# Kernel tuning notes

Measured on AMD Instinct MI355X. Metric: run time of the kernel, lower is better.

## Reference

```python
import jax, jax.numpy as jnp
import numpy as np

D_MODEL = 2048
NUM_HEADS = 16
HEAD_DIM = D_MODEL // NUM_HEADS
D_FF = 4 * D_MODEL
B, L = 2, 2048
LN_EPS = 1e-6


def layer_norm(x, scale, bias):
    x32 = x.astype(jnp.float32)
    mu = jnp.mean(x32, axis=-1, keepdims=True)
    var = jnp.mean(jnp.square(x32 - mu), axis=-1, keepdims=True)
    return (x32 - mu) * jax.lax.rsqrt(var + LN_EPS) * scale + bias


def setup_inputs() -> dict:
    key = jax.random.key(0)
    ks = jax.random.split(key, 10)
    s = 1.0 / np.sqrt(D_MODEL)
    x = jax.random.normal(ks[0], (B, L, D_MODEL), dtype=jnp.float32)
    mask = jnp.tril(jnp.ones((L, L), dtype=bool))[None, None, :, :]  # causal [1,1,L,L]
    wq = jax.random.normal(ks[1], (D_MODEL, D_MODEL), jnp.float32) * s
    wk = jax.random.normal(ks[2], (D_MODEL, D_MODEL), jnp.float32) * s
    wv = jax.random.normal(ks[3], (D_MODEL, D_MODEL), jnp.float32) * s
    wo = jax.random.normal(ks[4], (D_MODEL, D_MODEL), jnp.float32) * s
    w1 = jax.random.normal(ks[5], (D_MODEL, D_FF), jnp.float32) * s
    b1 = jnp.zeros((D_FF,), jnp.float32)
    w2 = jax.random.normal(ks[6], (D_FF, D_MODEL), jnp.float32) * (1.0 / np.sqrt(D_FF))
    b2 = jnp.zeros((D_MODEL,), jnp.float32)
    ln1_scale = jnp.ones((D_MODEL,), jnp.float32)
    ln1_bias = jnp.zeros((D_MODEL,), jnp.float32)
    ln2_scale = jnp.ones((D_MODEL,), jnp.float32)
    ln2_bias = jnp.zeros((D_MODEL,), jnp.float32)
    return {"x": x, "mask": mask, "ln1_scale": ln1_scale, "ln1_bias": ln1_bias,
            "wq": wq, "wk": wk, "wv": wv, "wo": wo,
            "ln2_scale": ln2_scale, "ln2_bias": ln2_bias,
            "w1": w1, "b1": b1, "w2": w2, "b2": b2}


def reference(x, mask, ln1_scale, ln1_bias, wq, wk, wv, wo,
              ln2_scale, ln2_bias, w1, b1, w2, b2):
    residual = x
    h = layer_norm(x, ln1_scale, ln1_bias)
    b, l, _ = h.shape
    q = (h @ wq).reshape(b, l, NUM_HEADS, HEAD_DIM)
    k = (h @ wk).reshape(b, l, NUM_HEADS, HEAD_DIM)
    v = (h @ wv).reshape(b, l, NUM_HEADS, HEAD_DIM)
    scores = jnp.einsum('bqhd,bkhd->bhqk', q, k) / jnp.sqrt(jnp.float32(HEAD_DIM))
    scores = jnp.where(mask, scores, -100000.0)
    attn = jax.nn.softmax(scores, axis=-1)
    attn_out = jnp.einsum('bhqk,bkhd->bqhd', attn, v).reshape(b, l, D_MODEL)
    x = residual + attn_out @ wo
    mlp = jax.nn.gelu(layer_norm(x, ln2_scale, ln2_bias) @ w1 + b1)
    return x + mlp @ w2 + b2
```

## Files before the change

kernel.cpp:

```cpp
#include <hip/hip_runtime.h>
#include <hip/hip_bf16.h>

typedef unsigned short u16;
typedef __bf16 bf16x8 __attribute__((ext_vector_type(8)));
typedef float f32x4 __attribute__((ext_vector_type(4)));

#define D_MODEL 2048
#define D_FF    8192
#define NH      16
#define HD      128
#define BATCH   2
#define SEQ     2048
#define ROWS    (BATCH*SEQ)

__device__ __forceinline__ u16 f2bf(float f) {
  union { __hip_bfloat16 h; u16 u; } cv;
  cv.h = __float2bfloat16(f);
  return cv.u;
}

__device__ __forceinline__ void gload16(const u16* g, u16* l) {
  __builtin_amdgcn_global_load_lds((const __attribute__((address_space(1))) void*)g,
                                   (__attribute__((address_space(3))) void*)l,
                                   16, 0, 0);
}

__device__ __forceinline__ float gelu_f(float x) {
  const float k0 = 0.7978845608028654f, k1 = 0.044715f;
  return 0.5f * x * (1.0f + tanhf(k0 * (x + k1 * x * x * x)));
}

__global__ __launch_bounds__(256) void ln_bf16_kernel(
    const float* __restrict__ x, const float* __restrict__ sc,
    const float* __restrict__ bs, u16* __restrict__ out)
{
  __shared__ float red[8];
  const int row = blockIdx.x, t = threadIdx.x;
  const int w = t >> 6, l = t & 63;
  const float* xr = x + (size_t)row * D_MODEL;
  float4 a = ((const float4*)xr)[t*2];
  float4 b = ((const float4*)xr)[t*2+1];
  float s  = a.x+a.y+a.z+a.w + b.x+b.y+b.z+b.w;
  float s2 = a.x*a.x+a.y*a.y+a.z*a.z+a.w*a.w + b.x*b.x+b.y*b.y+b.z*b.z+b.w*b.w;
  for (int off = 32; off; off >>= 1) { s += __shfl_down(s, off); s2 += __shfl_down(s2, off); }
  if (l == 0) { red[w] = s; red[4+w] = s2; }
  __syncthreads();
  s  = red[0]+red[1]+red[2]+red[3];
  s2 = red[4]+red[5]+red[6]+red[7];
  const float mu  = s * (1.0f / D_MODEL);
  const float var = s2 * (1.0f / D_MODEL) - mu * mu;
  const float inv = rsqrtf(var + 1e-6f);
  float4 g0 = ((const float4*)sc)[t*2], g1 = ((const float4*)sc)[t*2+1];
  float4 q0 = ((const float4*)bs)[t*2], q1 = ((const float4*)bs)[t*2+1];
  union { u16 u[8]; uint4 v; } o;
  o.u[0] = f2bf((a.x-mu)*inv*g0.x + q0.x);
  o.u[1] = f2bf((a.y-mu)*inv*g0.y + q0.y);
  o.u[2] = f2bf((a.z-mu)*inv*g0.z + q0.z);
  o.u[3] = f2bf((a.w-mu)*inv*g0.w + q0.w);
  o.u[4] = f2bf((b.x-mu)*inv*g1.x + q1.x);
  o.u[5] = f2bf((b.y-mu)*inv*g1.y + q1.y);
  o.u[6] = f2bf((b.z-mu)*inv*g1.z + q1.z);
  o.u[7] = f2bf((b.w-mu)*inv*g1.w + q1.w);
  *(uint4*)(&out[(size_t)row * D_MODEL + t*8]) = o.v;
}

__global__ __launch_bounds__(256) void transpose_w(
    const float* __restrict__ in, u16* __restrict__ out, int R, int C)
{
  __shared__ float tile[32][33];
  const int t = threadIdx.x;
  const int c0 = blockIdx.x*32, r0 = blockIdx.y*32;
  const int col = t & 31, rb = t >> 5;
#pragma unroll
  for (int i = 0; i < 4; ++i)
    tile[rb + i*8][col] = in[(size_t)(r0 + rb + i*8)*C + c0 + col];
  __syncthreads();
#pragma unroll
  for (int i = 0; i < 4; ++i)
    out[(size_t)(c0 + rb + i*8)*R + r0 + col] = f2bf(tile[col][rb + i*8]);
}

__global__ __launch_bounds__(256) void transpose_v(
    const u16* __restrict__ qkv, u16* __restrict__ vt)
{
  __shared__ u16 tile[32][34];
  const int t = threadIdx.x;
  const int b = blockIdx.z;
  const int c0 = blockIdx.x*32, r0 = blockIdx.y*32;
  const int col = t & 31, rb = t >> 5;
  const u16* inb = qkv + (size_t)b*SEQ*3*D_MODEL + 2*D_MODEL;
#pragma unroll
  for (int i = 0; i < 4; ++i)
    tile[rb+i*8][col] = inb[(size_t)(r0+rb+i*8)*(3*D_MODEL) + c0+col];
  __syncthreads();
  u16* ob = vt + (size_t)b*SEQ*D_MODEL;
#pragma unroll
  for (int i = 0; i < 4; ++i)
    ob[(size_t)(c0+rb+i*8)*SEQ + r0+col] = tile[col][rb+i*8];
}

template<int EPI>
__global__ __launch_bounds__(256) void gemm_bt(
    const u16* __restrict__ A, const u16* __restrict__ BT,
    void* __restrict__ Cout, const float* __restrict__ bias,
    const float* __restrict__ res, int N, int K)
{
  __shared__ u16 As[128*64];
  __shared__ u16 Bs[128*64];
  const int t = threadIdx.x;
  const int m0 = blockIdx.y*128, n0 = blockIdx.x*128;
  const int l = t & 63, w = t >> 6;
  const int wr = w >> 1, wc = w & 1;
  const int l15 = l & 15, lq = l >> 4;
  f32x4 acc[4][4] = {};

  for (int kt = 0; kt < K; kt += 64) {
    __syncthreads();
#pragma unroll
    for (int i = 0; i < 4; ++i) {
      const int o16 = i*256 + t;
      const int row = o16 >> 3, cs = o16 & 7;
      const int srcc = cs ^ (row & 7);
      gload16(A  + (size_t)(m0+row)*K + kt + srcc*8, &As[o16*8]);
      gload16(BT + (size_t)(n0+row)*K + kt + srcc*8, &Bs[o16*8]);
    }
    __syncthreads();
#pragma unroll
    for (int kk = 0; kk < 2; ++kk) {
      bf16x8 af[4], bfr[4];
#pragma unroll
      for (int mi = 0; mi < 4; ++mi) {
        const int r = wr*64 + mi*16 + l15;
        af[mi] = *(const bf16x8*)&As[r*64 + ((kk*4+lq) ^ (r&7))*8];
      }
#pragma unroll
      for (int ni = 0; ni < 4; ++ni) {
        const int r = wc*64 + ni*16 + l15;
        bfr[ni] = *(const bf16x8*)&Bs[r*64 + ((kk*4+lq) ^ (r&7))*8];
      }
#pragma unroll
      for (int mi = 0; mi < 4; ++mi)
#pragma unroll
        for (int ni = 0; ni < 4; ++ni)
          acc[mi][ni] = __builtin_amdgcn_mfma_f32_16x16x32_bf16(af[mi], bfr[ni], acc[mi][ni], 0, 0, 0);
    }
  }

  const int colb = n0 + wc*64;
  const int rowb = m0 + wr*64;
#pragma unroll
  for (int mi = 0; mi < 4; ++mi) {
#pragma unroll
    for (int ni = 0; ni < 4; ++ni) {
      const int col = colb + ni*16 + l15;
      const int row0 = rowb + mi*16 + lq*4;
      float bv = 0.f;
      if (EPI == 2 || EPI == 3) bv = bias[col];
#pragma unroll
      for (int r = 0; r < 4; ++r) {
        float v = acc[mi][ni][r];
        const size_t idx = (size_t)(row0 + r) * N + col;
        if (EPI == 0)      ((u16*)Cout)[idx] = f2bf(v);
        else if (EPI == 1) ((float*)Cout)[idx] = v + res[idx];
        else if (EPI == 2) ((u16*)Cout)[idx] = f2bf(gelu_f(v + bv));
        else               ((float*)Cout)[idx] = v + bv + res[idx];
      }
    }
  }
}

__global__ __launch_bounds__(256) void attn_kernel(
    const u16* __restrict__ qkv, const u16* __restrict__ vt,
    u16* __restrict__ out)
{
  __shared__ u16 Ks[64*128];
  __shared__ u16 Vs[128*64];
  __shared__ u16 Ps[4*16*64];
  const int t = threadIdx.x;
  const int qt = blockIdx.x & 31, bh = blockIdx.x >> 5;
  const int b = bh >> 4, h = bh & 15;
  const int w = t >> 6, l = t & 63;
  const int l15 = l & 15, lq = l >> 4;

  bf16x8 qf[4];
  {
    const u16* qb = qkv + (size_t)(b*SEQ + qt*64 + w*16 + l15)*(3*D_MODEL) + h*HD;
#pragma unroll
    for (int kk = 0; kk < 4; ++kk)
      qf[kk] = *(const bf16x8*)(qb + kk*32 + lq*8);
  }
  float m[4]    = {-INFINITY, -INFINITY, -INFINITY, -INFINITY};
  float lsum[4] = {0.f, 0.f, 0.f, 0.f};
  f32x4 acc_o[8] = {};
  const size_t kbase = (size_t)b*SEQ*(3*D_MODEL) + D_MODEL + h*HD;
  const size_t vbase = (size_t)(b*SEQ + h*HD) * SEQ;
  u16* pw = &Ps[w*1024];

  for (int j = 0; j <= qt; ++j) {
    __syncthreads();
#pragma unroll
    for (int i = 0; i < 4; ++i) {
      const int o16 = i*256 + t;
      {
        const int row = o16 >> 4, cs = o16 & 15;
        const int srcc = cs ^ (row & 7);
        gload16(qkv + kbase + (size_t)(j*64+row)*(3*D_MODEL) + srcc*8, &Ks[o16*8]);
      }
      {
        const int row = o16 >> 3, cs = o16 & 7;
        const int srcc = cs ^ (row & 7);
        gload16(vt + vbase + (size_t)row*SEQ + j*64 + srcc*8, &Vs[o16*8]);
      }
    }
    __syncthreads();

    f32x4 sacc[4] = {};
#pragma unroll
    for (int nf = 0; nf < 4; ++nf) {
      const int kr = nf*16 + l15;
      const int sw = kr & 7;
#pragma unroll
      for (int kk = 0; kk < 4; ++kk) {
        bf16x8 kf = *(const bf16x8*)&Ks[kr*128 + ((kk*4+lq) ^ sw)*8];
        sacc[nf] = __builtin_amdgcn_mfma_f32_16x16x32_bf16(qf[kk], kf, sacc[nf], 0, 0, 0);
      }
    }

    const float scale = 0.08838834764831845f;
    if (j == qt) {
#pragma unroll
      for (int nf = 0; nf < 4; ++nf)
#pragma unroll
        for (int r = 0; r < 4; ++r) {
          float s = sacc[nf][r] * scale;
          const int ki = nf*16 + l15;
          const int qi = w*16 + lq*4 + r;
          if (ki > qi) s = -100000.0f;
          sacc[nf][r] = s;
        }
    } else {
#pragma unroll
      for (int nf = 0; nf < 4; ++nf)
#pragma unroll
        for (int r = 0; r < 4; ++r) sacc[nf][r] *= scale;
    }

    float scal[4];
#pragma unroll
    for (int r = 0; r < 4; ++r) {
      float mx = fmaxf(fmaxf(sacc[0][r], sacc[1][r]), fmaxf(sacc[2][r], sacc[3][r]));
#pragma unroll
      for (int off = 1; off < 16; off <<= 1)
        mx = fmaxf(mx, __shfl_xor(mx, off));
      const float mn = fmaxf(m[r], mx);
      scal[r] = __expf(m[r] - mn);
      m[r] = mn;
      float rs = 0.f;
#pragma unroll
      for (int nf = 0; nf < 4; ++nf) {
        const float p = __expf(sacc[nf][r] - mn);
        sacc[nf][r] = p;
        rs += p;
      }
#pragma unroll
      for (int off = 1; off < 16; off <<= 1)
        rs += __shfl_xor(rs, off);
      lsum[r] = lsum[r]*scal[r] + rs;
    }
#pragma unroll
    for (int nf2 = 0; nf2 < 8; ++nf2)
#pragma unroll
      for (int r = 0; r < 4; ++r) acc_o[nf2][r] *= scal[r];

#pragma unroll
    for (int nf = 0; nf < 4; ++nf)
#pragma unroll
      for (int r = 0; r < 4; ++r) {
        const int qr = lq*4 + r, kc = nf*16 + l15;
        pw[qr*64 + (((kc>>3) ^ (qr&7))*8 + (kc&7))] = f2bf(sacc[nf][r]);
      }

#pragma unroll
    for (int kk2 = 0; kk2 < 2; ++kk2) {
      bf16x8 pf = *(const bf16x8*)&pw[l15*64 + (((kk2*4+lq) ^ (l15&7))*8)];
#pragma unroll
      for (int nf2 = 0; nf2 < 8; ++nf2) {
        const int vr = nf2*16 + l15;
        bf16x8 vf = *(const bf16x8*)&Vs[vr*64 + ((kk2*4+lq) ^ (vr&7))*8];
        acc_o[nf2] = __builtin_amdgcn_mfma_f32_16x16x32_bf16(pf, vf, acc_o[nf2], 0, 0, 0);
      }
    }
  }

  const size_t ro = (size_t)(b*SEQ + qt*64 + w*16 + lq*4);
#pragma unroll
  for (int r = 0; r < 4; ++r) {
    const float inv = 1.0f / lsum[r];
#pragma unroll
    for (int nf2 = 0; nf2 < 8; ++nf2)
      out[(ro + r)*D_MODEL + h*HD + nf2*16 + l15] = f2bf(acc_o[nf2][r] * inv);
  }
}

extern "C" void kernel_launch(void* const* d_in, const int* in_sizes, int n_in,
                              void* d_out, int out_size, void* d_ws, size_t ws_size,
                              hipStream_t stream)
{
  (void)in_sizes; (void)n_in; (void)out_size; (void)ws_size;
  const float* x    = (const float*)d_in[0];
  const float* ln1s = (const float*)d_in[2];
  const float* ln1b = (const float*)d_in[3];
  const float* wq   = (const float*)d_in[4];
  const float* wk   = (const float*)d_in[5];
  const float* wv   = (const float*)d_in[6];
  const float* wo   = (const float*)d_in[7];
  const float* ln2s = (const float*)d_in[8];
  const float* ln2b = (const float*)d_in[9];
  const float* w1   = (const float*)d_in[10];
  const float* b1   = (const float*)d_in[11];
  const float* w2   = (const float*)d_in[12];
  const float* b2   = (const float*)d_in[13];
  float* out = (float*)d_out;

  char* ws = (char*)d_ws;
  constexpr size_t OFF_WQKV = 0;
  constexpr size_t OFF_WO   = OFF_WQKV + (size_t)3*D_MODEL*D_MODEL*2;
  constexpr size_t OFF_W1   = OFF_WO   + (size_t)D_MODEL*D_MODEL*2;
  constexpr size_t OFF_W2   = OFF_W1   + (size_t)D_FF*D_MODEL*2;
  constexpr size_t OFF_H    = OFF_W2   + (size_t)D_MODEL*D_FF*2;
  constexpr size_t OFF_QKV  = OFF_H    + (size_t)ROWS*D_MODEL*2;
  constexpr size_t OFF_VT   = OFF_QKV  + (size_t)ROWS*3*D_MODEL*2;
  constexpr size_t OFF_ATTN = OFF_VT   + (size_t)ROWS*D_MODEL*2;
  constexpr size_t OFF_X2   = OFF_ATTN + (size_t)ROWS*D_MODEL*2;

  u16*   wqkv_bt = (u16*)(ws + OFF_WQKV);
  u16*   wo_bt   = (u16*)(ws + OFF_WO);
  u16*   w1_bt   = (u16*)(ws + OFF_W1);
  u16*   w2_bt   = (u16*)(ws + OFF_W2);
  u16*   h_bf    = (u16*)(ws + OFF_H);
  u16*   qkv     = (u16*)(ws + OFF_QKV);
  u16*   vt      = (u16*)(ws + OFF_VT);
  u16*   act     = qkv;
  u16*   attn    = (u16*)(ws + OFF_ATTN);
  float* x2      = (float*)(ws + OFF_X2);

  const dim3 B256(256);

  transpose_w<<<dim3(64,64),  B256, 0, stream>>>(wq, wqkv_bt,                 D_MODEL, D_MODEL);
  transpose_w<<<dim3(64,64),  B256, 0, stream>>>(wk, wqkv_bt + (size_t)D_MODEL*D_MODEL,   D_MODEL, D_MODEL);
  transpose_w<<<dim3(64,64),  B256, 0, stream>>>(wv, wqkv_bt + (size_t)2*D_MODEL*D_MODEL, D_MODEL, D_MODEL);
  transpose_w<<<dim3(64,64),  B256, 0, stream>>>(wo, wo_bt, D_MODEL, D_MODEL);
  transpose_w<<<dim3(256,64), B256, 0, stream>>>(w1, w1_bt, D_MODEL, D_FF);
  transpose_w<<<dim3(64,256), B256, 0, stream>>>(w2, w2_bt, D_FF, D_MODEL);

  ln_bf16_kernel<<<ROWS, B256, 0, stream>>>(x, ln1s, ln1b, h_bf);
  gemm_bt<0><<<dim3(48,32), B256, 0, stream>>>(h_bf, wqkv_bt, qkv, nullptr, nullptr, 3*D_MODEL, D_MODEL);
  transpose_v<<<dim3(64,64,2), B256, 0, stream>>>(qkv, vt);
  attn_kernel<<<dim3(BATCH*NH*32), B256, 0, stream>>>(qkv, vt, attn);
  gemm_bt<1><<<dim3(16,32), B256, 0, stream>>>(attn, wo_bt, x2, nullptr, x, D_MODEL, D_MODEL);
  ln_bf16_kernel<<<ROWS, B256, 0, stream>>>(x2, ln2s, ln2b, h_bf);
  gemm_bt<2><<<dim3(64,32), B256, 0, stream>>>(h_bf, w1_bt, act, b1, nullptr, D_FF, D_MODEL);
  gemm_bt<3><<<dim3(16,32), B256, 0, stream>>>(act, w2_bt, out, b2, x2, D_MODEL, D_FF);
}
```

Baseline: 769.7 us.

## Replace GEMM with 256-tile multi-stage pipelined kernels and XCD-aware block remap

Replaces the single 128x128 GEMM with two variants: a 256x256 tile kernel for the QKV and W1 GEMMs and a 256x128 kernel for the Wo and W2 GEMMs. Both use 512 threads and a 4-buffer LDS ring with 3 tiles of global->LDS prefetch in flight. They split the MFMA work into halves interleaved with the loads, use explicit waitcnt/barriers and setprio around MFMA bursts, and remap block IDs across the 8 XCDs for L2 locality. The aim is to hide global-memory latency and raise arithmetic intensity per block. In exchange it uses more LDS and registers, and relies on hand-placed waitcnt counts being correct.

New measurement: 719.4 us. -6.5%, faster.

```diff
diff --git a/kernel.cpp b/kernel.cpp
--- a/kernel.cpp
+++ b/kernel.cpp
@@ -100,70 +100,200 @@
 }
 
 template<int EPI>
-__global__ __launch_bounds__(256) void gemm_bt(
+__global__ __launch_bounds__(512, 2) void gemm256(
     const u16* __restrict__ A, const u16* __restrict__ BT,
     void* __restrict__ Cout, const float* __restrict__ bias,
-    const float* __restrict__ res, int N, int K)
-{
-  __shared__ u16 As[128*64];
-  __shared__ u16 Bs[128*64];
+    int N, int K, int gridN)
+{
+  __shared__ __align__(16) u16 lds[65536];
   const int t = threadIdx.x;
-  const int m0 = blockIdx.y*128, n0 = blockIdx.x*128;
-  const int l = t & 63, w = t >> 6;
-  const int wr = w >> 1, wc = w & 1;
+  const int nwg = gridDim.x;
+  const int wg = (int)blockIdx.x;
+  const int wgid = (wg & 7) * (nwg >> 3) + (wg >> 3);
+  const int bx = wgid % gridN, by = wgid / gridN;
+  const int m0 = by * 256, n0 = bx * 256;
+  const int w = t >> 6, l = t & 63;
+  const int wm = w >> 2, wn = w & 3;
   const int l15 = l & 15, lq = l >> 4;
+
+  const int o0 = t, o1 = 512 + t;
+  const int r0 = o0 >> 2, c0s = (o0 & 3) ^ ((r0 >> 1) & 3);
+  const int r1 = o1 >> 2, c1s = (o1 & 3) ^ ((r1 >> 1) & 3);
+  const u16* a0 = A  + (size_t)(m0 + r0) * K + c0s * 8;
+  const u16* a1 = A  + (size_t)(m0 + r1) * K + c1s * 8;
+  const u16* b0 = BT + (size_t)(n0 + r0) * K + c0s * 8;
+  const u16* b1 = BT + (size_t)(n0 + r1) * K + c1s * 8;
+
+  int offA[4], offA2[4], offB[4];
+#pragma unroll
+  for (int i = 0; i < 4; ++i) {
+    const int ra  = wm * 128 + i * 16 + l15;
+    offA[i]  = ra * 32 + ((lq ^ ((ra >> 1) & 3)) * 8);
+    const int ra2 = ra + 64;
+    offA2[i] = ra2 * 32 + ((lq ^ ((ra2 >> 1) & 3)) * 8);
+    const int rb  = wn * 64 + i * 16 + l15;
+    offB[i]  = 8192 + rb * 32 + ((lq ^ ((rb >> 1) & 3)) * 8);
+  }
+
+  f32x4 acc[8][4] = {};
+  const int nt = K >> 5;
+
+#define STAGE_A(tile) { u16* d = &lds[((tile) & 3) * 16384]; \
+    gload16(a0 + (size_t)(tile) * 32, d + o0 * 8); \
+    gload16(a1 + (size_t)(tile) * 32, d + o1 * 8); }
+#define STAGE_B(tile) { u16* d = &lds[((tile) & 3) * 16384 + 8192]; \
+    gload16(b0 + (size_t)(tile) * 32, d + o0 * 8); \
+    gload16(b1 + (size_t)(tile) * 32, d + o1 * 8); }
+
+  STAGE_A(0); STAGE_B(0); STAGE_A(1); STAGE_B(1); STAGE_A(2); STAGE_B(2);
+  asm volatile("s_waitcnt vmcnt(8)" ::: "memory");
+  __builtin_amdgcn_sched_barrier(0);
+  __builtin_amdgcn_s_barrier();
+
+  for (int tt = 0; tt < nt; ++tt) {
+    u16* buf = &lds[(tt & 3) * 16384];
+    bf16x8 af[4], bfr[4];
+#pragma unroll
+    for (int i = 0; i < 4; ++i) af[i]  = *(const bf16x8*)&buf[offA[i]];
+#pragma unroll
+    for (int i = 0; i < 4; ++i) bfr[i] = *(const bf16x8*)&buf[offB[i]];
+    if (tt + 3 < nt) STAGE_A(tt + 3);
+    __builtin_amdgcn_s_barrier();
+    asm volatile("s_waitcnt lgkmcnt(0)" ::: "memory");
+    __builtin_amdgcn_sched_barrier(0);
+    __builtin_amdgcn_s_setprio(1);
+#pragma unroll
+    for (int mi = 0; mi < 4; ++mi)
+#pragma unroll
+      for (int ni = 0; ni < 4; ++ni)
+        acc[mi][ni] = __builtin_amdgcn_mfma_f32_16x16x32_bf16(af[mi], bfr[ni], acc[mi][ni], 0, 0, 0);
+    __builtin_amdgcn_s_setprio(0);
+    __builtin_amdgcn_s_barrier();
+    bf16x8 af2[4];
+#pragma unroll
+    for (int i = 0; i < 4; ++i) af2[i] = *(const bf16x8*)&buf[offA2[i]];
+    if (tt + 3 < nt) STAGE_B(tt + 3);
+    __builtin_amdgcn_s_barrier();
+    asm volatile("s_waitcnt lgkmcnt(0)" ::: "memory");
+    __builtin_amdgcn_sched_barrier(0);
+    __builtin_amdgcn_s_setprio(1);
+#pragma unroll
+    for (int mi = 0; mi < 4; ++mi)
+#pragma unroll
+      for (int ni = 0; ni < 4; ++ni)
+        acc[4 + mi][ni] = __builtin_amdgcn_mfma_f32_16x16x32_bf16(af2[mi], bfr[ni], acc[4 + mi][ni], 0, 0, 0);
+    __builtin_amdgcn_s_setprio(0);
+    asm volatile("s_waitcnt vmcnt(8)" ::: "memory");
+    __builtin_amdgcn_sched_barrier(0);
+    __builtin_amdgcn_s_barrier();
+  }
+#undef STAGE_A
+#undef STAGE_B
+
+  const int rowb = m0 + wm * 128;
+  const int colb = n0 + wn * 64;
+#pragma unroll
+  for (int mi = 0; mi < 8; ++mi) {
+#pragma unroll
+    for (int ni = 0; ni < 4; ++ni) {
+      const int col = colb + ni * 16 + l15;
+      const int row0 = rowb + mi * 16 + lq * 4;
+      float bv = (EPI == 2) ? bias[col] : 0.f;
+#pragma unroll
+      for (int r = 0; r < 4; ++r) {
+        const float v = acc[mi][ni][r];
+        const size_t idx = (size_t)(row0 + r) * N + col;
+        if (EPI == 0) ((u16*)Cout)[idx] = f2bf(v);
+        else          ((u16*)Cout)[idx] = f2bf(gelu_f(v + bv));
+      }
+    }
+  }
+}
+
+template<int EPI>
+__global__ __launch_bounds__(512, 2) void gemm128(
+    const u16* __restrict__ A, const u16* __restrict__ BT,
+    float* __restrict__ Cout, const float* __restrict__ bias,
+    const float* __restrict__ res, int N, int K, int gridN)
+{
+  __shared__ __align__(16) u16 lds[49152];
+  const int t = threadIdx.x;
+  const int nwg = gridDim.x;
+  const int wg = (int)blockIdx.x;
+  const int wgid = (wg & 7) * (nwg >> 3) + (wg >> 3);
+  const int bx = wgid % gridN, by = wgid / gridN;
+  const int m0 = by * 256, n0 = bx * 128;
+  const int w = t >> 6, l = t & 63;
+  const int wm = w >> 1, wn = w & 1;
+  const int l15 = l & 15, lq = l >> 4;
+
+  const int o0 = t, o1 = 512 + t;
+  const int r0 = o0 >> 2, c0s = (o0 & 3) ^ ((r0 >> 1) & 3);
+  const int r1 = o1 >> 2, c1s = (o1 & 3) ^ ((r1 >> 1) & 3);
+  const u16* a0 = A  + (size_t)(m0 + r0) * K + c0s * 8;
+  const u16* a1 = A  + (size_t)(m0 + r1) * K + c1s * 8;
+  const u16* bsrc = BT + (size_t)(n0 + r0) * K + c0s * 8;
+
+  int offA[4], offB[4];
+#pragma unroll
+  for (int i = 0; i < 4; ++i) {
+    const int ra = wm * 64 + i * 16 + l15;
+    offA[i] = ra * 32 + ((lq ^ ((ra >> 1) & 3)) * 8);
+    const int rb = wn * 64 + i * 16 + l15;
+    offB[i] = 8192 + rb * 32 + ((lq ^ ((rb >> 1) & 3)) * 8);
+  }
+
   f32x4 acc[4][4] = {};
-
-  for (int kt = 0; kt < K; kt += 64) {
-    __syncthreads();
-#pragma unroll
-    for (int i = 0; i < 4; ++i) {
-      const int o16 = i*256 + t;
-      const int row = o16 >> 3, cs = o16 & 7;
-      const int srcc = cs ^ (row & 7);
-      gload16(A  + (size_t)(m0+row)*K + kt + srcc*8, &As[o16*8]);
-      gload16(BT + (size_t)(n0+row)*K + kt + srcc*8, &Bs[o16*8]);
-    }
-    __syncthreads();
-#pragma unroll
-    for (int kk = 0; kk < 2; ++kk) {
-      bf16x8 af[4], bfr[4];
-#pragma unroll
-      for (int mi = 0; mi < 4; ++mi) {
-        const int r = wr*64 + mi*16 + l15;
-        af[mi] = *(const bf16x8*)&As[r*64 + ((kk*4+lq) ^ (r&7))*8];
-      }
-#pragma unroll
-      for (int ni = 0; ni < 4; ++ni) {
-        const int r = wc*64 + ni*16 + l15;
-        bfr[ni] = *(const bf16x8*)&Bs[r*64 + ((kk*4+lq) ^ (r&7))*8];
-      }
-#pragma unroll
-      for (int mi = 0; mi < 4; ++mi)
-#pragma unroll
-        for (int ni = 0; ni < 4; ++ni)
-          acc[mi][ni] = __builtin_amdgcn_mfma_f32_16x16x32_bf16(af[mi], bfr[ni], acc[mi][ni], 0, 0, 0);
-    }
-  }
-
-  const int colb = n0 + wc*64;
-  const int rowb = m0 + wr*64;
+  const int nt = K >> 5;
+
+#define STAGE(tile) { u16* d = &lds[((tile) & 3) * 12288]; \
+    gload16(a0 + (size_t)(tile) * 32, d + o0 * 8); \
+    gload16(a1 + (size_t)(tile) * 32, d + o1 * 8); \
+    gload16(bsrc + (size_t)(tile) * 32, d + 8192 + o0 * 8); }
+
+  STAGE(0); STAGE(1); STAGE(2);
+  asm volatile("s_waitcnt vmcnt(6)" ::: "memory");
+  __builtin_amdgcn_sched_barrier(0);
+  __builtin_amdgcn_s_barrier();
+
+  for (int tt = 0; tt < nt; ++tt) {
+    u16* buf = &lds[(tt & 3) * 12288];
+    bf16x8 af[4], bfr[4];
+#pragma unroll
+    for (int i = 0; i < 4; ++i) af[i]  = *(const bf16x8*)&buf[offA[i]];
+#pragma unroll
+    for (int i = 0; i < 4; ++i) bfr[i] = *(const bf16x8*)&buf[offB[i]];
+    if (tt + 3 < nt) STAGE(tt + 3);
+    __builtin_amdgcn_s_barrier();
+    asm volatile("s_waitcnt lgkmcnt(0)" ::: "memory");
+    __builtin_amdgcn_sched_barrier(0);
+    __builtin_amdgcn_s_setprio(1);
+#pragma unroll
+    for (int mi = 0; mi < 4; ++mi)
+#pragma unroll
+      for (int ni = 0; ni < 4; ++ni)
+        acc[mi][ni] = __builtin_amdgcn_mfma_f32_16x16x32_bf16(af[mi], bfr[ni], acc[mi][ni], 0, 0, 0);
+    __builtin_amdgcn_s_setprio(0);
+    asm volatile("s_waitcnt vmcnt(6)" ::: "memory");
+    __builtin_amdgcn_sched_barrier(0);
+    __builtin_amdgcn_s_barrier();
+  }
+#undef STAGE
+
+  const int rowb = m0 + wm * 64;
+  const int colb = n0 + wn * 64;
 #pragma unroll
   for (int mi = 0; mi < 4; ++mi) {
 #pragma unroll
     for (int ni = 0; ni < 4; ++ni) {
-      const int col = colb + ni*16 + l15;
-      const int row0 = rowb + mi*16 + lq*4;
-      float bv = 0.f;
-      if (EPI == 2 || EPI == 3) bv = bias[col];
+      const int col = colb + ni * 16 + l15;
+      const int row0 = rowb + mi * 16 + lq * 4;
+      float bv = (EPI == 3) ? bias[col] : 0.f;
 #pragma unroll
       for (int r = 0; r < 4; ++r) {
-        float v = acc[mi][ni][r];
+        const float v = acc[mi][ni][r];
         const size_t idx = (size_t)(row0 + r) * N + col;
-        if (EPI == 0)      ((u16*)Cout)[idx] = f2bf(v);
-        else if (EPI == 1) ((float*)Cout)[idx] = v + res[idx];
-        else if (EPI == 2) ((u16*)Cout)[idx] = f2bf(gelu_f(v + bv));
-        else               ((float*)Cout)[idx] = v + bv + res[idx];
+        Cout[idx] = v + bv + res[idx];
       }
     }
   }
@@ -344,7 +474,7 @@
   u16*   attn    = (u16*)(ws + OFF_ATTN);
   float* x2      = (float*)(ws + OFF_X2);
 
-  const dim3 B256(256);
+  const dim3 B256(256), B512(512);
 
   transpose_w<<<dim3(64,64),  B256, 0, stream>>>(wq, wqkv_bt,                 D_MODEL, D_MODEL);
   transpose_w<<<dim3(64,64),  B256, 0, stream>>>(wk, wqkv_bt + (size_t)D_MODEL*D_MODEL,   D_MODEL, D_MODEL);
@@ -354,11 +484,11 @@
   transpose_w<<<dim3(64,256), B256, 0, stream>>>(w2, w2_bt, D_FF, D_MODEL);
 
   ln_bf16_kernel<<<ROWS, B256, 0, stream>>>(x, ln1s, ln1b, h_bf);
-  gemm_bt<0><<<dim3(48,32), B256, 0, stream>>>(h_bf, wqkv_bt, qkv, nullptr, nullptr, 3*D_MODEL, D_MODEL);
+  gemm256<0><<<dim3(384), B512, 0, stream>>>(h_bf, wqkv_bt, qkv, nullptr, 3*D_MODEL, D_MODEL, 24);
   transpose_v<<<dim3(64,64,2), B256, 0, stream>>>(qkv, vt);
   attn_kernel<<<dim3(BATCH*NH*32), B256, 0, stream>>>(qkv, vt, attn);
-  gemm_bt<1><<<dim3(16,32), B256, 0, stream>>>(attn, wo_bt, x2, nullptr, x, D_MODEL, D_MODEL);
+  gemm128<1><<<dim3(256), B512, 0, stream>>>(attn, wo_bt, x2, nullptr, x, D_MODEL, D_MODEL, 16);
   ln_bf16_kernel<<<ROWS, B256, 0, stream>>>(x2, ln2s, ln2b, h_bf);
-  gemm_bt<2><<<dim3(64,32), B256, 0, stream>>>(h_bf, w1_bt, act, b1, nullptr, D_FF, D_MODEL);
-  gemm_bt<3><<<dim3(16,32), B256, 0, stream>>>(act, w2_bt, out, b2, x2, D_MODEL, D_FF);
-}
+  gemm256<2><<<dim3(512), B512, 0, stream>>>(h_bf, w1_bt, act, b1, D_FF, D_MODEL, 32);
+  gemm128<3><<<dim3(256), B512, 0, stream>>>(act, w2_bt, out, b2, x2, D_MODEL, D_FF, 16);
+}
```

## Pipeline GEMM with four-stage LDS ring buffer and XCD-aware block remapping

Applied to the files above, without the earlier changes.

Replaces the single-buffered 128x128x64 GEMM with a 4-deep LDS ring of 32-wide K tiles. Loads are issued three tiles ahead and gated by vmcnt waits, so global loads overlap the MFMA work. It also adds a 1D grid with block-id remapping across the 8 XCDs for L2 locality, setprio around the MFMAs, and 2 blocks per CU via launch bounds. The cost is more LDS per block (64KB), which may limit occupancy, and delicate barrier and waitcnt ordering.

New measurement: 772.7 us. Within noise of the previous version (+0.4%).

```diff
diff --git a/kernel.cpp b/kernel.cpp
--- a/kernel.cpp
+++ b/kernel.cpp
@@ -100,65 +100,95 @@
 }
 
 template<int EPI>
-__global__ __launch_bounds__(256) void gemm_bt(
+__global__ __launch_bounds__(256, 2) void gemm_p4(
     const u16* __restrict__ A, const u16* __restrict__ BT,
     void* __restrict__ Cout, const float* __restrict__ bias,
-    const float* __restrict__ res, int N, int K)
-{
-  __shared__ u16 As[128*64];
-  __shared__ u16 Bs[128*64];
+    const float* __restrict__ res, int N, int K, int gridN)
+{
+  __shared__ __align__(16) u16 lds[32768];
   const int t = threadIdx.x;
-  const int m0 = blockIdx.y*128, n0 = blockIdx.x*128;
-  const int l = t & 63, w = t >> 6;
-  const int wr = w >> 1, wc = w & 1;
+  const int nwg = gridDim.x;
+  const int wg = (int)blockIdx.x;
+  const int wgid = (wg & 7) * (nwg >> 3) + (wg >> 3);
+  const int bx = wgid % gridN, by = wgid / gridN;
+  const int m0 = by * 128, n0 = bx * 128;
+  const int w = t >> 6, l = t & 63;
+  const int wm = w >> 1, wn = w & 1;
   const int l15 = l & 15, lq = l >> 4;
+
+  const int o0 = t, o1 = 256 + t;
+  const int r0 = o0 >> 2, c0s = (o0 & 3) ^ ((r0 >> 1) & 3);
+  const int r1 = o1 >> 2, c1s = (o1 & 3) ^ ((r1 >> 1) & 3);
+  const u16* a0 = A  + (size_t)(m0 + r0) * K + c0s * 8;
+  const u16* a1 = A  + (size_t)(m0 + r1) * K + c1s * 8;
+  const u16* b0 = BT + (size_t)(n0 + r0) * K + c0s * 8;
+  const u16* b1 = BT + (size_t)(n0 + r1) * K + c1s * 8;
+
+  int offA[4], offB[4];
+#pragma unroll
+  for (int i = 0; i < 4; ++i) {
+    const int ra = wm * 64 + i * 16 + l15;
+    offA[i] = ra * 32 + ((lq ^ ((ra >> 1) & 3)) * 8);
+    const int rb = wn * 64 + i * 16 + l15;
+    offB[i] = 4096 + rb * 32 + ((lq ^ ((rb >> 1) & 3)) * 8);
+  }
+
   f32x4 acc[4][4] = {};
-
-  for (int kt = 0; kt < K; kt += 64) {
-    __syncthreads();
-#pragma unroll
-    for (int i = 0; i < 4; ++i) {
-      const int o16 = i*256 + t;
-      const int row = o16 >> 3, cs = o16 & 7;
-      const int srcc = cs ^ (row & 7);
-      gload16(A  + (size_t)(m0+row)*K + kt + srcc*8, &As[o16*8]);
-      gload16(BT + (size_t)(n0+row)*K + kt + srcc*8, &Bs[o16*8]);
-    }
-    __syncthreads();
-#pragma unroll
-    for (int kk = 0; kk < 2; ++kk) {
-      bf16x8 af[4], bfr[4];
-#pragma unroll
-      for (int mi = 0; mi < 4; ++mi) {
-        const int r = wr*64 + mi*16 + l15;
-        af[mi] = *(const bf16x8*)&As[r*64 + ((kk*4+lq) ^ (r&7))*8];
-      }
-#pragma unroll
-      for (int ni = 0; ni < 4; ++ni) {
-        const int r = wc*64 + ni*16 + l15;
-        bfr[ni] = *(const bf16x8*)&Bs[r*64 + ((kk*4+lq) ^ (r&7))*8];
-      }
-#pragma unroll
-      for (int mi = 0; mi < 4; ++mi)
-#pragma unroll
-        for (int ni = 0; ni < 4; ++ni)
-          acc[mi][ni] = __builtin_amdgcn_mfma_f32_16x16x32_bf16(af[mi], bfr[ni], acc[mi][ni], 0, 0, 0);
-    }
-  }
-
-  const int colb = n0 + wc*64;
-  const int rowb = m0 + wr*64;
+  const int nt = K >> 5;
+
+#define STAGE(tile) { u16* d = &lds[((tile) & 3) * 8192]; \
+    gload16(a0 + (size_t)(tile) * 32, d + o0 * 8); \
+    gload16(a1 + (size_t)(tile) * 32, d + o1 * 8); \
+    gload16(b0 + (size_t)(tile) * 32, d + 4096 + o0 * 8); \
+    gload16(b1 + (size_t)(tile) * 32, d + 4096 + o1 * 8); }
+
+#define KSTEP(TT, DOSTAGE, VMSTR) { \
+    u16* buf = &lds[((TT) & 3) * 8192]; \
+    if (DOSTAGE) STAGE((TT) + 3); \
+    bf16x8 af[4], bfr[4]; \
+    _Pragma("unroll") \
+    for (int i = 0; i < 4; ++i) af[i]  = *(const bf16x8*)&buf[offA[i]]; \
+    _Pragma("unroll") \
+    for (int i = 0; i < 4; ++i) bfr[i] = *(const bf16x8*)&buf[offB[i]]; \
+    __builtin_amdgcn_s_barrier(); \
+    asm volatile("s_waitcnt lgkmcnt(0)" ::: "memory"); \
+    __builtin_amdgcn_sched_barrier(0); \
+    __builtin_amdgcn_s_setprio(1); \
+    _Pragma("unroll") \
+    for (int mi = 0; mi < 4; ++mi) \
+      _Pragma("unroll") \
+      for (int ni = 0; ni < 4; ++ni) \
+        acc[mi][ni] = __builtin_amdgcn_mfma_f32_16x16x32_bf16(af[mi], bfr[ni], acc[mi][ni], 0, 0, 0); \
+    __builtin_amdgcn_s_setprio(0); \
+    asm volatile("s_waitcnt " VMSTR ::: "memory"); \
+    __builtin_amdgcn_sched_barrier(0); \
+    __builtin_amdgcn_s_barrier(); }
+
+  STAGE(0); STAGE(1); STAGE(2);
+  asm volatile("s_waitcnt vmcnt(8)" ::: "memory");
+  __builtin_amdgcn_sched_barrier(0);
+  __builtin_amdgcn_s_barrier();
+
+  for (int tt = 0; tt < nt - 3; ++tt)
+    KSTEP(tt, true, "vmcnt(8)")
+  KSTEP(nt - 3, false, "vmcnt(4)")
+  KSTEP(nt - 2, false, "vmcnt(0)")
+  KSTEP(nt - 1, false, "vmcnt(0)")
+#undef KSTEP
+#undef STAGE
+
+  const int rowb = m0 + wm * 64;
+  const int colb = n0 + wn * 64;
 #pragma unroll
   for (int mi = 0; mi < 4; ++mi) {
 #pragma unroll
     for (int ni = 0; ni < 4; ++ni) {
-      const int col = colb + ni*16 + l15;
-      const int row0 = rowb + mi*16 + lq*4;
-      float bv = 0.f;
-      if (EPI == 2 || EPI == 3) bv = bias[col];
+      const int col = colb + ni * 16 + l15;
+      const int row0 = rowb + mi * 16 + lq * 4;
+      float bv = (EPI == 2 || EPI == 3) ? bias[col] : 0.f;
 #pragma unroll
       for (int r = 0; r < 4; ++r) {
-        float v = acc[mi][ni][r];
+        const float v = acc[mi][ni][r];
         const size_t idx = (size_t)(row0 + r) * N + col;
         if (EPI == 0)      ((u16*)Cout)[idx] = f2bf(v);
         else if (EPI == 1) ((float*)Cout)[idx] = v + res[idx];
@@ -354,11 +384,11 @@
   transpose_w<<<dim3(64,256), B256, 0, stream>>>(w2, w2_bt, D_FF, D_MODEL);
 
   ln_bf16_kernel<<<ROWS, B256, 0, stream>>>(x, ln1s, ln1b, h_bf);
-  gemm_bt<0><<<dim3(48,32), B256, 0, stream>>>(h_bf, wqkv_bt, qkv, nullptr, nullptr, 3*D_MODEL, D_MODEL);
+  gemm_p4<0><<<dim3(1536), B256, 0, stream>>>(h_bf, wqkv_bt, qkv, nullptr, nullptr, 3*D_MODEL, D_MODEL, 48);
   transpose_v<<<dim3(64,64,2), B256, 0, stream>>>(qkv, vt);
   attn_kernel<<<dim3(BATCH*NH*32), B256, 0, stream>>>(qkv, vt, attn);
-  gemm_bt<1><<<dim3(16,32), B256, 0, stream>>>(attn, wo_bt, x2, nullptr, x, D_MODEL, D_MODEL);
+  gemm_p4<1><<<dim3(512), B256, 0, stream>>>(attn, wo_bt, (void*)x2, nullptr, x, D_MODEL, D_MODEL, 16);
   ln_bf16_kernel<<<ROWS, B256, 0, stream>>>(x2, ln2s, ln2b, h_bf);
-  gemm_bt<2><<<dim3(64,32), B256, 0, stream>>>(h_bf, w1_bt, act, b1, nullptr, D_FF, D_MODEL);
-  gemm_bt<3><<<dim3(16,32), B256, 0, stream>>>(act, w2_bt, out, b2, x2, D_MODEL, D_FF);
-}
+  gemm_p4<2><<<dim3(2048), B256, 0, stream>>>(h_bf, w1_bt, act, b1, nullptr, D_FF, D_MODEL, 64);
+  gemm_p4<3><<<dim3(512), B256, 0, stream>>>(act, w2_bt, (void*)out, b2, x2, D_MODEL, D_FF, 16);
+}
```
